# Kernel optimization log

Hardware: AMD Instinct MI355X
Metric: run time of the kernel (lower is better)

## Reference

```python
import jax, jax.numpy as jnp
import numpy as np

EPS = 1e-7  # keras K.epsilon()
ROUTINGS = 3


def squash(v, axis=-1):
    s = jnp.sum(v * v, axis=axis, keepdims=True)
    scale = s / (1.0 + s) / jnp.sqrt(s + EPS)
    return scale * v


def setup_inputs() -> dict:
    key = jax.random.key(0)
    k1, k2 = jax.random.split(key)
    B, I, K = 256, 2048, 8   # batch, input_num_capsule, input_dim_capsule
    J, D = 10, 16            # num_capsule, dim_capsule
    inputs = jax.random.normal(k1, (B, I, K), dtype=jnp.float32)
    W = jax.random.normal(k2, (J, I, D, K), dtype=jnp.float32) * 0.05
    return {"inputs": inputs, "W": W}


def reference(inputs, W):
    # inputs: [B, I, K]; W: [J, I, D, K]
    # inputs_hat[b,j,i,d] = W[j,i] @ inputs[b,i]  -> [B, J, I, D]
    u_hat = jnp.einsum('jidk,bik->bjid', W, inputs)
    B, J, I, _ = u_hat.shape
    b = jnp.zeros((B, J, 1, I), dtype=u_hat.dtype)
    outputs = None
    for r in range(ROUTINGS):
        c = jax.nn.softmax(b, axis=1)                       # softmax over output capsules
        s = jnp.einsum('bjqi,bjid->bjqd', c, u_hat)          # [B, J, 1, D]
        outputs = squash(s, axis=-1)
        if r < ROUTINGS - 1:
            b = b + jnp.einsum('bjqd,bjid->bjqi', outputs, u_hat)
    return jnp.squeeze(outputs, axis=2)                      # [B, J, D]
```

## Files before the change

### kernel.cpp

```cpp
#include <hip/hip_runtime.h>
#include <math.h>


#define BB 256
#define II 2048
#define KK 8
#define JJ 10
#define DD 16

typedef __attribute__((ext_vector_type(4))) float f32x4;
typedef __attribute__((ext_vector_type(8))) short short8;

__device__ __forceinline__ short f2bf(float f) {
    union { float f; unsigned u; } v; v.f = f;
    unsigned r = v.u + 0x7FFFu + ((v.u >> 16) & 1u);
    return (short)(r >> 16);
}

__device__ __forceinline__ void gload16(const short* g, short* l) {
    __builtin_amdgcn_global_load_lds(
        (const __attribute__((address_space(1))) unsigned int*)g,
        (__attribute__((address_space(3))) unsigned int*)l,
        16, 0, 0);
}

__global__ __launch_bounds__(256) void pre_kernel(const float* __restrict__ x,
                                                  const float* __restrict__ W,
                                                  short* __restrict__ xTb,
                                                  short* __restrict__ Wb) {
    __shared__ float4 tile[8 * 66];
    const int t = threadIdx.x;
    const int bid = blockIdx.x;
    if (bid < 1280) {
        const int idx = bid * 256 + t;
        const float4* src = (const float4*)(W + (size_t)idx * 8);
        const float4 a = src[0], b = src[1];
        short8 o;
        o[0] = f2bf(a.x); o[1] = f2bf(a.y); o[2] = f2bf(a.z); o[3] = f2bf(a.w);
        o[4] = f2bf(b.x); o[5] = f2bf(b.y); o[6] = f2bf(b.z); o[7] = f2bf(b.w);
        *(short8*)(Wb + (size_t)idx * 8) = o;
    } else {
        const int bb = bid - 1280;
        const int b0 = (bb >> 8) * 32, i0 = (bb & 255) * 8;
        {
            const int lb = t >> 3, li = t & 7;
            const float4* src = (const float4*)(x + ((b0 + lb) * II + (i0 + li)) * KK);
            tile[li * 66 + lb * 2 + 0] = src[0];
            tile[li * 66 + lb * 2 + 1] = src[1];
        }
        __syncthreads();
        {
            const int ri = t >> 5, rb = t & 31;
            const float4 p0 = tile[ri * 66 + rb * 2 + 0];
            const float4 p1 = tile[ri * 66 + rb * 2 + 1];
            short8 o;
            o[0] = f2bf(p0.x); o[1] = f2bf(p0.y); o[2] = f2bf(p0.z); o[3] = f2bf(p0.w);
            o[4] = f2bf(p1.x); o[5] = f2bf(p1.y); o[6] = f2bf(p1.z); o[7] = f2bf(p1.w);
            *(short8*)(xTb + ((size_t)(i0 + ri) * BB + (b0 + rb)) * KK) = o;
        }
    }
}

#define LBUF 14336

__device__ __forceinline__ void seg_src_dst(int s, int i0, int b0,
                                            const short* __restrict__ xTb,
                                            const short* __restrict__ Wb,
                                            const short** src, int* dst) {
    if (s < 20) {
        const int j = s >> 1, h = s & 1;
        *src = Wb + ((size_t)(j * II + i0) * DD) * KK + h * 512;
        *dst = j * 1024 + h * 512;
    } else {
        const int il = s - 20;
        *src = xTb + ((size_t)(i0 + il) * BB + b0) * KK;
        *dst = 10240 + il * 512;
    }
}

template <int USE_C>
__global__ __launch_bounds__(256) void round_mfma(
    const short* __restrict__ xTb, const short* __restrict__ Wb,
    const float* __restrict__ vT, _Float16* __restrict__ p)
{
    __shared__ short L[2][LBUF];
    const int t = threadIdx.x;
    const int lane = t & 63, wv = t >> 6;
    const int col = lane & 15, q = lane >> 4;
    const int b0 = blockIdx.y * 64;
    const int bl = wv * 16 + col;
    const int i0 = blockIdx.x * 16;

#pragma unroll
    for (int n = 0; n < 7; ++n) {
        const int s = wv + n * 4;
        const short* src; int dst;
        seg_src_dst(s, i0, b0, xTb, Wb, &src, &dst);
        gload16(src + lane * 8, &L[0][dst]);
        seg_src_dst(s, i0 + 8, b0, xTb, Wb, &src, &dst);
        gload16(src + lane * 8, &L[1][dst]);
    }

    float vfrag[JJ][4];
    if (USE_C) {
#pragma unroll
        for (int j = 0; j < JJ; ++j)
#pragma unroll
            for (int r = 0; r < 4; ++r)
                vfrag[j][r] = vT[(j * DD + q * 4 + r) * BB + b0 + bl];
    }

    __syncthreads();

    f32x4 sfrag[JJ];
#pragma unroll
    for (int j = 0; j < JJ; ++j) sfrag[j] = (f32x4){0.f, 0.f, 0.f, 0.f};

#pragma unroll
    for (int sc = 0; sc < 2; ++sc) {
        const short* Lb = L[sc];
        if (USE_C) {
#pragma unroll 2
            for (int il = 0; il < 8; ++il) {
                short8 A[JJ], Bf;
                const short8 z = (short8){0, 0, 0, 0, 0, 0, 0, 0};
                Bf = z;
#pragma unroll
                for (int j = 0; j < JJ; ++j) A[j] = z;
                if (q == 0) {
                    Bf = *(const short8*)(&Lb[10240 + il * 512 + bl * 8]);
#pragma unroll
                    for (int j = 0; j < JJ; ++j)
                        A[j] = *(const short8*)(&Lb[j * 1024 + il * 128 + col * 8]);
                }
                f32x4 U[JJ];
#pragma unroll
                for (int j = 0; j < JJ; ++j)
                    U[j] = __builtin_amdgcn_mfma_f32_16x16x32_bf16(
                        A[j], Bf, (f32x4){0.f, 0.f, 0.f, 0.f}, 0, 0, 0);
                float Lg[JJ];
#pragma unroll
                for (int j = 0; j < JJ; ++j)
                    Lg[j] = vfrag[j][0] * U[j][0] + vfrag[j][1] * U[j][1]
                          + vfrag[j][2] * U[j][2] + vfrag[j][3] * U[j][3];
#pragma unroll
                for (int j = 0; j < JJ; ++j) {
                    Lg[j] += __shfl_xor(Lg[j], 16, 64);
                    Lg[j] += __shfl_xor(Lg[j], 32, 64);
                }
                float sum = 0.f;
#pragma unroll
                for (int j = 0; j < JJ; ++j) { Lg[j] = __expf(Lg[j]); sum += Lg[j]; }
                const float inv = __builtin_amdgcn_rcpf(sum);
#pragma unroll
                for (int j = 0; j < JJ; ++j) {
                    const float c = Lg[j] * inv;
#pragma unroll
                    for (int r = 0; r < 4; ++r) sfrag[j][r] += c * U[j][r];
                }
            }
        } else {
#pragma unroll
            for (int s = 0; s < 2; ++s) {
                const int il = s * 4 + q;
                const short8 Bf = *(const short8*)(&Lb[10240 + il * 512 + bl * 8]);
#pragma unroll
                for (int j = 0; j < JJ; ++j) {
                    const short8 A = *(const short8*)(&Lb[j * 1024 + il * 128 + col * 8]);
                    sfrag[j] = __builtin_amdgcn_mfma_f32_16x16x32_bf16(A, Bf, sfrag[j], 0, 0, 0);
                }
            }
        }
    }

    _Float16* pp = p + ((size_t)(blockIdx.y * 4 + wv) * 128 + blockIdx.x) * (JJ * 256);
#pragma unroll
    for (int j = 0; j < JJ; ++j) {
        union { uint2 u; _Float16 h[4]; } pk;
        pk.h[0] = (_Float16)sfrag[j][0];
        pk.h[1] = (_Float16)sfrag[j][1];
        pk.h[2] = (_Float16)sfrag[j][2];
        pk.h[3] = (_Float16)sfrag[j][3];
        *(uint2*)(pp + (size_t)(j * 64 + lane) * 4) = pk.u;
    }
}

template <int MODE>
__global__ __launch_bounds__(512) void rs_kernel(const _Float16* __restrict__ p,
                                                 float* __restrict__ vT,
                                                 float* __restrict__ out, float scale) {
    __shared__ f32x4 red[512];
    const int t = threadIdx.x;
    const int j = blockIdx.x, bt = blockIdx.y;
    const int eg = t & 63, cg = t >> 6;

    const _Float16* pp = p + ((size_t)bt * 128 + cg * 16) * (JJ * 256) + j * 256 + eg * 4;
    float s0 = 0.f, s1 = 0.f, s2 = 0.f, s3 = 0.f;
#pragma unroll 8
    for (int ch = 0; ch < 16; ++ch) {
        union { uint2 u; _Float16 h[4]; } cv;
        cv.u = *(const uint2*)(pp + (size_t)ch * (JJ * 256));
        s0 += (float)cv.h[0]; s1 += (float)cv.h[1];
        s2 += (float)cv.h[2]; s3 += (float)cv.h[3];
    }
    red[t] = (f32x4){s0, s1, s2, s3};
    __syncthreads();
    if (t < 64) {
        f32x4 a = red[t];
#pragma unroll
        for (int g = 1; g < 8; ++g) a += red[64 * g + t];
        const float x0 = a[0] * scale, x1 = a[1] * scale;
        const float x2 = a[2] * scale, x3 = a[3] * scale;
        float ss = x0 * x0 + x1 * x1 + x2 * x2 + x3 * x3;
        ss += __shfl_xor(ss, 16, 64);
        ss += __shfl_xor(ss, 32, 64);
        const float coef = ss / (1.f + ss) / sqrtf(ss + 1e-7f);
        const int qd = t >> 4, bc = t & 15;
        const float v[4] = {coef * x0, coef * x1, coef * x2, coef * x3};
#pragma unroll
        for (int r = 0; r < 4; ++r) {
            const int d = qd * 4 + r;
            if (MODE == 0) vT[(j * DD + d) * BB + bt * 16 + bc] = v[r];
            if (MODE == 1) vT[(j * DD + d) * BB + bt * 16 + bc] += v[r];
            if (MODE == 2) out[((bt * 16 + bc) * JJ + j) * DD + d] = v[r];
        }
    }
}

#define IT_OLD 32
#define BT_OLD 16

__global__ __launch_bounds__(256) void zero_kernel(float* __restrict__ p, int n) {
    int idx = blockIdx.x * blockDim.x + threadIdx.x;
    if (idx < n) p[idx] = 0.f;
}

__global__ __launch_bounds__(256) void squash_old(float* __restrict__ s_acc,
                                                  float* __restrict__ dst, float scale,
                                                  int add_to_dst, int zero_src) {
    int idx = blockIdx.x * blockDim.x + threadIdx.x;
    if (idx >= BB * JJ) return;
    float s[DD];
    float ss = 0.f;
#pragma unroll
    for (int d = 0; d < DD; ++d) {
        s[d] = s_acc[idx * DD + d] * scale;
        ss += s[d] * s[d];
    }
    const float coef = ss / (1.f + ss) / sqrtf(ss + 1e-7f);
#pragma unroll
    for (int d = 0; d < DD; ++d) {
        const float vv = coef * s[d];
        if (add_to_dst) dst[idx * DD + d] += vv;
        else            dst[idx * DD + d] = vv;
        if (zero_src)   s_acc[idx * DD + d] = 0.f;
    }
}

__global__ __launch_bounds__(256) void round1_old(const float* __restrict__ x,
                                                  const float* __restrict__ W,
                                                  float* __restrict__ s_acc) {
    const int t = threadIdx.x;
    const int d = t & 15;
    const int bq = t >> 4;
    const int b = blockIdx.y * BT_OLD + bq;
    const int i0 = blockIdx.x * IT_OLD;
    float acc[JJ];
#pragma unroll
    for (int j = 0; j < JJ; ++j) acc[j] = 0.f;
    for (int ii = 0; ii < IT_OLD; ++ii) {
        const int i = i0 + ii;
        const float* xp = x + ((b * II) + i) * KK;
        const float4 xa = *(const float4*)(xp);
        const float4 xb = *(const float4*)(xp + 4);
#pragma unroll
        for (int j = 0; j < JJ; ++j) {
            const float* wp = W + (((j * II + i) * DD + d) * KK);
            const float4 w0 = *(const float4*)(wp);
            const float4 w1 = *(const float4*)(wp + 4);
            acc[j] += w0.x*xa.x + w0.y*xa.y + w0.z*xa.z + w0.w*xa.w
                    + w1.x*xb.x + w1.y*xb.y + w1.z*xb.z + w1.w*xb.w;
        }
    }
#pragma unroll
    for (int j = 0; j < JJ; ++j)
        atomicAdd(&s_acc[(b * JJ + j) * DD + d], acc[j]);
}

__global__ __launch_bounds__(256) void round_old(const float* __restrict__ x,
                                                 const float* __restrict__ W,
                                                 const float* __restrict__ v,
                                                 float* __restrict__ s_acc) {
    const int t = threadIdx.x;
    const int d = t & 15;
    const int bq = t >> 4;
    const int b = blockIdx.y * BT_OLD + bq;
    const int i0 = blockIdx.x * IT_OLD;
    float vr[JJ], acc[JJ];
#pragma unroll
    for (int j = 0; j < JJ; ++j) {
        vr[j] = v[(b * JJ + j) * DD + d];
        acc[j] = 0.f;
    }
    for (int ii = 0; ii < IT_OLD; ++ii) {
        const int i = i0 + ii;
        const float* xp = x + ((b * II) + i) * KK;
        const float4 xa = *(const float4*)(xp);
        const float4 xb = *(const float4*)(xp + 4);
        float U[JJ], Lg[JJ];
#pragma unroll
        for (int j = 0; j < JJ; ++j) {
            const float* wp = W + (((j * II + i) * DD + d) * KK);
            const float4 w0 = *(const float4*)(wp);
            const float4 w1 = *(const float4*)(wp + 4);
            U[j] = w0.x*xa.x + w0.y*xa.y + w0.z*xa.z + w0.w*xa.w
                 + w1.x*xb.x + w1.y*xb.y + w1.z*xb.z + w1.w*xb.w;
            Lg[j] = vr[j] * U[j];
        }
#pragma unroll
        for (int m = 8; m >= 1; m >>= 1) {
#pragma unroll
            for (int j = 0; j < JJ; ++j) Lg[j] += __shfl_xor(Lg[j], m, 64);
        }
        float mx = Lg[0];
#pragma unroll
        for (int j = 1; j < JJ; ++j) mx = fmaxf(mx, Lg[j]);
        float sum = 0.f;
#pragma unroll
        for (int j = 0; j < JJ; ++j) { Lg[j] = __expf(Lg[j] - mx); sum += Lg[j]; }
        const float inv = 1.f / sum;
#pragma unroll
        for (int j = 0; j < JJ; ++j) acc[j] += (Lg[j] * inv) * U[j];
    }
#pragma unroll
    for (int j = 0; j < JJ; ++j)
        atomicAdd(&s_acc[(b * JJ + j) * DD + d], acc[j]);
}

extern "C" void kernel_launch(void* const* d_in, const int* in_sizes, int n_in,
                              void* d_out, int out_size, void* d_ws, size_t ws_size,
                              hipStream_t stream) {
    const float* x = (const float*)d_in[0];
    const float* W = (const float*)d_in[1];
    float* out = (float*)d_out;

    float* vT     = (float*)d_ws;
    _Float16* p   = (_Float16*)(vT + BB * JJ * DD);
    short* xTb    = (short*)(p + (size_t)16 * 128 * 2560);
    short* Wb     = xTb + (size_t)II * BB * KK;
    const size_t need = (size_t)(BB * JJ * DD) * 4
                      + (size_t)16 * 128 * 2560 * 2
                      + ((size_t)II * BB * KK + (size_t)JJ * II * DD * KK) * 2;

    if (ws_size >= need) {
        pre_kernel<<<1280 + 2048, 256, 0, stream>>>(x, W, xTb, Wb);

        dim3 rg(128, 4);
        dim3 sg(JJ, 16);
        round_mfma<0><<<rg, 256, 0, stream>>>(xTb, Wb, vT, p);
        rs_kernel<0><<<sg, 512, 0, stream>>>(p, vT, out, 0.1f);
        round_mfma<1><<<rg, 256, 0, stream>>>(xTb, Wb, vT, p);
        rs_kernel<1><<<sg, 512, 0, stream>>>(p, vT, out, 1.0f);
        round_mfma<1><<<rg, 256, 0, stream>>>(xTb, Wb, vT, p);
        rs_kernel<2><<<sg, 512, 0, stream>>>(p, vT, out, 1.0f);
    } else {
        float* s_acc = (float*)d_ws;
        float* v_buf = s_acc + BB * JJ * DD;
        const int NS = BB * JJ * DD;
        dim3 rg(II / IT_OLD, BB / BT_OLD);
        zero_kernel<<<(NS + 255) / 256, 256, 0, stream>>>(s_acc, NS);
        round1_old<<<rg, 256, 0, stream>>>(x, W, s_acc);
        squash_old<<<(BB * JJ + 255) / 256, 256, 0, stream>>>(s_acc, v_buf, 0.1f, 0, 1);
        round_old<<<rg, 256, 0, stream>>>(x, W, v_buf, s_acc);
        squash_old<<<(BB * JJ + 255) / 256, 256, 0, stream>>>(s_acc, v_buf, 1.0f, 1, 1);
        round_old<<<rg, 256, 0, stream>>>(x, W, v_buf, s_acc);
        squash_old<<<(BB * JJ + 255) / 256, 256, 0, stream>>>(s_acc, out, 1.0f, 0, 0);
    }
}
```

Before: 136.6 us.

## Fuse bf16 conversion of x and W into first routing round kernel

Removes the separate pre-kernel and instead has the first routing round read fp32 x and W, convert them to bf16 straight into LDS, and run the MFMA accumulation. The same block also writes the bf16 copies to global for later rounds, with W written only by the ytile==0 blocks. This saves one launch and a full read-back of the converted tensors. In exchange, W is read and converted four times (once per batch tile), and the loads are synchronous register loads rather than async LDS loads.

```diff
diff --git a/kernel.cpp b/kernel.cpp
--- a/kernel.cpp
+++ b/kernel.cpp
@@ -22,43 +22,6 @@
         (const __attribute__((address_space(1))) unsigned int*)g,
         (__attribute__((address_space(3))) unsigned int*)l,
         16, 0, 0);
-}
-
-__global__ __launch_bounds__(256) void pre_kernel(const float* __restrict__ x,
-                                                  const float* __restrict__ W,
-                                                  short* __restrict__ xTb,
-                                                  short* __restrict__ Wb) {
-    __shared__ float4 tile[8 * 66];
-    const int t = threadIdx.x;
-    const int bid = blockIdx.x;
-    if (bid < 1280) {
-        const int idx = bid * 256 + t;
-        const float4* src = (const float4*)(W + (size_t)idx * 8);
-        const float4 a = src[0], b = src[1];
-        short8 o;
-        o[0] = f2bf(a.x); o[1] = f2bf(a.y); o[2] = f2bf(a.z); o[3] = f2bf(a.w);
-        o[4] = f2bf(b.x); o[5] = f2bf(b.y); o[6] = f2bf(b.z); o[7] = f2bf(b.w);
-        *(short8*)(Wb + (size_t)idx * 8) = o;
-    } else {
-        const int bb = bid - 1280;
-        const int b0 = (bb >> 8) * 32, i0 = (bb & 255) * 8;
-        {
-            const int lb = t >> 3, li = t & 7;
-            const float4* src = (const float4*)(x + ((b0 + lb) * II + (i0 + li)) * KK);
-            tile[li * 66 + lb * 2 + 0] = src[0];
-            tile[li * 66 + lb * 2 + 1] = src[1];
-        }
-        __syncthreads();
-        {
-            const int ri = t >> 5, rb = t & 31;
-            const float4 p0 = tile[ri * 66 + rb * 2 + 0];
-            const float4 p1 = tile[ri * 66 + rb * 2 + 1];
-            short8 o;
-            o[0] = f2bf(p0.x); o[1] = f2bf(p0.y); o[2] = f2bf(p0.z); o[3] = f2bf(p0.w);
-            o[4] = f2bf(p1.x); o[5] = f2bf(p1.y); o[6] = f2bf(p1.z); o[7] = f2bf(p1.w);
-            *(short8*)(xTb + ((size_t)(i0 + ri) * BB + (b0 + rb)) * KK) = o;
-        }
-    }
 }
 
 #define LBUF 14336
@@ -78,7 +41,78 @@
     }
 }
 
-template <int USE_C>
+__global__ __launch_bounds__(256) void round1_fused(
+    const float* __restrict__ x, const float* __restrict__ W,
+    short* __restrict__ xTb, short* __restrict__ Wb, _Float16* __restrict__ p)
+{
+    __shared__ short L[2][LBUF];
+    const int t = threadIdx.x;
+    const int lane = t & 63, wv = t >> 6;
+    const int col = lane & 15, q = lane >> 4;
+    const int chunk = blockIdx.x, ytile = blockIdx.y;
+    const int b0 = ytile * 64;
+    const int bl = wv * 16 + col;
+    const int i0 = chunk * 16;
+
+#pragma unroll
+    for (int n = 0; n < 10; ++n) {
+        const int r = t + n * 256;
+        const int d = r & 15, i = (r >> 4) & 15, j = r >> 8;
+        const size_t off = ((size_t)(j * II + i0 + i) * DD + d) * KK;
+        const float4 a = *(const float4*)(W + off);
+        const float4 b = *(const float4*)(W + off + 4);
+        short8 o;
+        o[0] = f2bf(a.x); o[1] = f2bf(a.y); o[2] = f2bf(a.z); o[3] = f2bf(a.w);
+        o[4] = f2bf(b.x); o[5] = f2bf(b.y); o[6] = f2bf(b.z); o[7] = f2bf(b.w);
+        *(short8*)(&L[i >> 3][j * 1024 + (i & 7) * 128 + d * 8]) = o;
+        if (ytile == 0) *(short8*)(Wb + off) = o;
+    }
+#pragma unroll
+    for (int n = 0; n < 4; ++n) {
+        const int r = t + n * 256;
+        const int b = r & 63, i = r >> 6;
+        const float* xp = x + ((size_t)(b0 + b) * II + (i0 + i)) * KK;
+        const float4 a = *(const float4*)xp;
+        const float4 c = *(const float4*)(xp + 4);
+        short8 o;
+        o[0] = f2bf(a.x); o[1] = f2bf(a.y); o[2] = f2bf(a.z); o[3] = f2bf(a.w);
+        o[4] = f2bf(c.x); o[5] = f2bf(c.y); o[6] = f2bf(c.z); o[7] = f2bf(c.w);
+        *(short8*)(&L[i >> 3][10240 + (i & 7) * 512 + b * 8]) = o;
+        *(short8*)(xTb + ((size_t)(i0 + i) * BB + b0 + b) * KK) = o;
+    }
+    __syncthreads();
+
+    f32x4 sfrag[JJ];
+#pragma unroll
+    for (int j = 0; j < JJ; ++j) sfrag[j] = (f32x4){0.f, 0.f, 0.f, 0.f};
+
+#pragma unroll
+    for (int sc = 0; sc < 2; ++sc) {
+        const short* Lb = L[sc];
+#pragma unroll
+        for (int s = 0; s < 2; ++s) {
+            const int il = s * 4 + q;
+            const short8 Bf = *(const short8*)(&Lb[10240 + il * 512 + bl * 8]);
+#pragma unroll
+            for (int j = 0; j < JJ; ++j) {
+                const short8 A = *(const short8*)(&Lb[j * 1024 + il * 128 + col * 8]);
+                sfrag[j] = __builtin_amdgcn_mfma_f32_16x16x32_bf16(A, Bf, sfrag[j], 0, 0, 0);
+            }
+        }
+    }
+
+    _Float16* pp = p + ((size_t)(ytile * 4 + wv) * 128 + chunk) * (JJ * 256);
+#pragma unroll
+    for (int j = 0; j < JJ; ++j) {
+        union { uint2 u; _Float16 h[4]; } pk;
+        pk.h[0] = (_Float16)sfrag[j][0];
+        pk.h[1] = (_Float16)sfrag[j][1];
+        pk.h[2] = (_Float16)sfrag[j][2];
+        pk.h[3] = (_Float16)sfrag[j][3];
+        *(uint2*)(pp + (size_t)(j * 64 + lane) * 4) = pk.u;
+    }
+}
+
 __global__ __launch_bounds__(256) void round_mfma(
     const short* __restrict__ xTb, const short* __restrict__ Wb,
     const float* __restrict__ vT, _Float16* __restrict__ p)
@@ -102,13 +136,11 @@
     }
 
     float vfrag[JJ][4];
-    if (USE_C) {
-#pragma unroll
-        for (int j = 0; j < JJ; ++j)
-#pragma unroll
-            for (int r = 0; r < 4; ++r)
-                vfrag[j][r] = vT[(j * DD + q * 4 + r) * BB + b0 + bl];
-    }
+#pragma unroll
+    for (int j = 0; j < JJ; ++j)
+#pragma unroll
+        for (int r = 0; r < 4; ++r)
+            vfrag[j][r] = vT[(j * DD + q * 4 + r) * BB + b0 + bl];
 
     __syncthreads();
 
@@ -119,56 +151,43 @@
 #pragma unroll
     for (int sc = 0; sc < 2; ++sc) {
         const short* Lb = L[sc];
-        if (USE_C) {
 #pragma unroll 2
-            for (int il = 0; il < 8; ++il) {
-                short8 A[JJ], Bf;
-                const short8 z = (short8){0, 0, 0, 0, 0, 0, 0, 0};
-                Bf = z;
-#pragma unroll
-                for (int j = 0; j < JJ; ++j) A[j] = z;
-                if (q == 0) {
-                    Bf = *(const short8*)(&Lb[10240 + il * 512 + bl * 8]);
-#pragma unroll
-                    for (int j = 0; j < JJ; ++j)
-                        A[j] = *(const short8*)(&Lb[j * 1024 + il * 128 + col * 8]);
-                }
-                f32x4 U[JJ];
+        for (int il = 0; il < 8; ++il) {
+            short8 A[JJ], Bf;
+            const short8 z = (short8){0, 0, 0, 0, 0, 0, 0, 0};
+            Bf = z;
+#pragma unroll
+            for (int j = 0; j < JJ; ++j) A[j] = z;
+            if (q == 0) {
+                Bf = *(const short8*)(&Lb[10240 + il * 512 + bl * 8]);
 #pragma unroll
                 for (int j = 0; j < JJ; ++j)
-                    U[j] = __builtin_amdgcn_mfma_f32_16x16x32_bf16(
-                        A[j], Bf, (f32x4){0.f, 0.f, 0.f, 0.f}, 0, 0, 0);
-                float Lg[JJ];
-#pragma unroll
-                for (int j = 0; j < JJ; ++j)
-                    Lg[j] = vfrag[j][0] * U[j][0] + vfrag[j][1] * U[j][1]
-                          + vfrag[j][2] * U[j][2] + vfrag[j][3] * U[j][3];
-#pragma unroll
-                for (int j = 0; j < JJ; ++j) {
-                    Lg[j] += __shfl_xor(Lg[j], 16, 64);
-                    Lg[j] += __shfl_xor(Lg[j], 32, 64);
-                }
-                float sum = 0.f;
-#pragma unroll
-                for (int j = 0; j < JJ; ++j) { Lg[j] = __expf(Lg[j]); sum += Lg[j]; }
-                const float inv = __builtin_amdgcn_rcpf(sum);
-#pragma unroll
-                for (int j = 0; j < JJ; ++j) {
-                    const float c = Lg[j] * inv;
-#pragma unroll
-                    for (int r = 0; r < 4; ++r) sfrag[j][r] += c * U[j][r];
-                }
+                    A[j] = *(const short8*)(&Lb[j * 1024 + il * 128 + col * 8]);
             }
-        } else {
-#pragma unroll
-            for (int s = 0; s < 2; ++s) {
-                const int il = s * 4 + q;
-                const short8 Bf = *(const short8*)(&Lb[10240 + il * 512 + bl * 8]);
-#pragma unroll
-                for (int j = 0; j < JJ; ++j) {
-                    const short8 A = *(const short8*)(&Lb[j * 1024 + il * 128 + col * 8]);
-                    sfrag[j] = __builtin_amdgcn_mfma_f32_16x16x32_bf16(A, Bf, sfrag[j], 0, 0, 0);
-                }
+            f32x4 U[JJ];
+#pragma unroll
+            for (int j = 0; j < JJ; ++j)
+                U[j] = __builtin_amdgcn_mfma_f32_16x16x32_bf16(
+                    A[j], Bf, (f32x4){0.f, 0.f, 0.f, 0.f}, 0, 0, 0);
+            float Lg[JJ];
+#pragma unroll
+            for (int j = 0; j < JJ; ++j)
+                Lg[j] = vfrag[j][0] * U[j][0] + vfrag[j][1] * U[j][1]
+                      + vfrag[j][2] * U[j][2] + vfrag[j][3] * U[j][3];
+#pragma unroll
+            for (int j = 0; j < JJ; ++j) {
+                Lg[j] += __shfl_xor(Lg[j], 16, 64);
+                Lg[j] += __shfl_xor(Lg[j], 32, 64);
+            }
+            float sum = 0.f;
+#pragma unroll
+            for (int j = 0; j < JJ; ++j) { Lg[j] = __expf(Lg[j]); sum += Lg[j]; }
+            const float inv = __builtin_amdgcn_rcpf(sum);
+#pragma unroll
+            for (int j = 0; j < JJ; ++j) {
+                const float c = Lg[j] * inv;
+#pragma unroll
+                for (int r = 0; r < 4; ++r) sfrag[j][r] += c * U[j][r];
             }
         }
     }
@@ -353,15 +372,13 @@
                       + ((size_t)II * BB * KK + (size_t)JJ * II * DD * KK) * 2;
 
     if (ws_size >= need) {
-        pre_kernel<<<1280 + 2048, 256, 0, stream>>>(x, W, xTb, Wb);
-
         dim3 rg(128, 4);
         dim3 sg(JJ, 16);
-        round_mfma<0><<<rg, 256, 0, stream>>>(xTb, Wb, vT, p);
+        round1_fused<<<rg, 256, 0, stream>>>(x, W, xTb, Wb, p);
         rs_kernel<0><<<sg, 512, 0, stream>>>(p, vT, out, 0.1f);
-        round_mfma<1><<<rg, 256, 0, stream>>>(xTb, Wb, vT, p);
+        round_mfma<<<rg, 256, 0, stream>>>(xTb, Wb, vT, p);
         rs_kernel<1><<<sg, 512, 0, stream>>>(p, vT, out, 1.0f);
-        round_mfma<1><<<rg, 256, 0, stream>>>(xTb, Wb, vT, p);
+        round_mfma<<<rg, 256, 0, stream>>>(xTb, Wb, vT, p);
         rs_kernel<2><<<sg, 512, 0, stream>>>(p, vT, out, 1.0f);
     } else {
         float* s_acc = (float*)d_ws;
```

New measurement: 136.8 us. Within noise of the previous version (+0.1%).
